# Performance work log

Hardware: AMD Instinct MI355X
Metric: run time of the kernel (lower is better)

Reference implementation:

```python
import jax, jax.numpy as jnp
import numpy as np

N, E, DIN, DH, DOUT, G, H = 40000, 400000, 256, 128, 128, 256, 4
BN_EPS = 1e-5      # nn.BatchNorm1d default
SM_EPS = 1e-16     # PyG softmax eps
NEG_SLOPE = 0.2    # GATConv default negative_slope


def _gat(x, src, dst, W, a_src, a_dst, b, heads, out_ch):
    # x:[N,Fin] W:[Fin,heads*out_ch] a_*:[heads,out_ch] b:[out_ch]
    n = x.shape[0]
    h = (x @ W).reshape(n, heads, out_ch)                     # [N,H,C]
    e = (h * a_src).sum(-1)[src] + (h * a_dst).sum(-1)[dst]   # [E,H] attention logits
    e = jnp.where(e > 0, e, NEG_SLOPE * e)                    # leaky_relu
    m = jax.ops.segment_max(e, dst, num_segments=n)           # segment softmax over incoming edges
    p = jnp.exp(e - m[dst])
    z = jax.ops.segment_sum(p, dst, num_segments=n)
    alpha = p / (z[dst] + SM_EPS)                             # [E,H]
    out = jax.ops.segment_sum(h[src] * alpha[:, :, None], dst, num_segments=n)  # [N,H,C]
    return out.mean(axis=1) + b                               # concat=False -> mean over heads, then bias


def _bn(x, g, b, m, v):
    # eval-mode BatchNorm1d with running stats
    return (x - m) * jax.lax.rsqrt(v + BN_EPS) * g + b


def setup_inputs():
    key = jax.random.key(0)
    ks = jax.random.split(key, 16)
    def rn(k, shape, fan):
        return jax.random.normal(k, shape, jnp.float32) / np.sqrt(fan).astype(np.float32)
    return {
        "x": jax.random.normal(ks[0], (N, DIN), jnp.float32),
        "src": jax.random.randint(ks[1], (E,), 0, N),
        "dst": jax.random.randint(ks[2], (E,), 0, N),
        "batch": jnp.sort(jax.random.randint(ks[3], (N,), 0, G)),
        "W1": rn(ks[4], (DIN, H * DH), DIN), "as1": rn(ks[5], (H, DH), DH), "ad1": rn(ks[6], (H, DH), DH), "b1": jnp.zeros((DH,), jnp.float32),
        "g1": jnp.ones((DH,), jnp.float32), "be1": jnp.zeros((DH,), jnp.float32), "m1": jnp.zeros((DH,), jnp.float32), "v1": jnp.ones((DH,), jnp.float32),
        "W2": rn(ks[7], (DH, H * DH), DH), "as2": rn(ks[8], (H, DH), DH), "ad2": rn(ks[9], (H, DH), DH), "b2": jnp.zeros((DH,), jnp.float32),
        "g2": jnp.ones((DH,), jnp.float32), "be2": jnp.zeros((DH,), jnp.float32), "m2": jnp.zeros((DH,), jnp.float32), "v2": jnp.ones((DH,), jnp.float32),
        "W3": rn(ks[10], (DH, DOUT), DH), "as3": rn(ks[11], (1, DOUT), DOUT), "ad3": rn(ks[12], (1, DOUT), DOUT), "b3": jnp.zeros((DOUT,), jnp.float32),
    }


def reference(x, src, dst, batch, W1, as1, ad1, b1, g1, be1, m1, v1,
              W2, as2, ad2, b2, g2, be2, m2, v2, W3, as3, ad3, b3):
    n = x.shape[0]
    loop = jnp.arange(n)
    s = jnp.concatenate([src, loop])  # PyG GATConv add_self_loops=True
    d = jnp.concatenate([dst, loop])
    h = jax.nn.elu(_gat(x, s, d, W1, as1, ad1, b1, H, DH))
    h = _bn(h, g1, be1, m1, v1)
    h = jax.nn.elu(_gat(h, s, d, W2, as2, ad2, b2, H, DH))
    h = _bn(h, g2, be2, m2, v2)
    h = _gat(h, s, d, W3, as3, ad3, b3, 1, DOUT)
    tot = jax.ops.segment_sum(h, batch, num_segments=G)      # global_mean_pool
    cnt = jax.ops.segment_sum(jnp.ones((n,), h.dtype), batch, num_segments=G)
    return tot / jnp.maximum(cnt, 1.0)[:, None]
```

## Files before the change

kernel.cpp:

```cpp
#include <hip/hip_runtime.h>
#include <cstdint>

#define N_NODES 40000
#define N_EDGES 400000
#define DIN 256
#define DHID 128
#define NG 256
#define NHEAD 4
#define ETOT (N_EDGES + N_NODES)

typedef __attribute__((ext_vector_type(8))) short short8;
typedef __attribute__((ext_vector_type(8))) unsigned short bfx8;
typedef __attribute__((ext_vector_type(4))) unsigned short bfx4;
typedef __attribute__((ext_vector_type(4))) float floatx4;

static __device__ __forceinline__ unsigned short f2bf(float f) {
    unsigned u = __float_as_uint(f);
    unsigned r = (u + 0x7FFFu + ((u >> 16) & 1u)) >> 16;
    return (unsigned short)r;
}
static __device__ __forceinline__ float bf2f(unsigned short s) {
    return __uint_as_float((unsigned)s << 16);
}


__global__ void count_kernel(const int* __restrict__ dst, int* __restrict__ deg) {
    int i = blockIdx.x * 256 + threadIdx.x;
    if (i >= ETOT) return;
    int d = (i < N_EDGES) ? dst[i] : (i - N_EDGES);
    atomicAdd(&deg[d], 1);
}

__global__ __launch_bounds__(1024) void scan_kernel(const int* __restrict__ deg,
                                                    int* __restrict__ offs,
                                                    int* __restrict__ cursor) {
    const int VPT = 40;
    __shared__ int wsum[16];
    int t = threadIdx.x;
    int lane = t & 63, wv = t >> 6;
    int base = t * VPT;
    int vals[VPT];
    int run = 0;
#pragma unroll
    for (int i = 0; i < VPT; i++) {
        int idx = base + i;
        int v = (idx < N_NODES) ? deg[idx] : 0;
        vals[i] = run;
        run += v;
    }
    int inc = run;
#pragma unroll
    for (int off = 1; off < 64; off <<= 1) {
        int n = __shfl_up(inc, off, 64);
        if (lane >= off) inc += n;
    }
    if (lane == 63) wsum[wv] = inc;
    __syncthreads();
    if (t == 0) {
        int c = 0;
#pragma unroll
        for (int i = 0; i < 16; i++) { int v = wsum[i]; wsum[i] = c; c += v; }
    }
    __syncthreads();
    int excl = wsum[wv] + inc - run;
#pragma unroll
    for (int i = 0; i < VPT; i++) {
        int idx = base + i;
        if (idx < N_NODES) { int o = excl + vals[i]; offs[idx] = o; cursor[idx] = o; }
    }
    if (t == 0) offs[N_NODES] = ETOT;
}

__global__ void fill_kernel(const int* __restrict__ src, const int* __restrict__ dst,
                            int* __restrict__ cursor, int* __restrict__ csr) {
    int i = blockIdx.x * 256 + threadIdx.x;
    if (i >= ETOT) return;
    int s, d;
    if (i < N_EDGES) { s = src[i]; d = dst[i]; } else { s = d = i - N_EDGES; }
    int pos = atomicAdd(&cursor[d], 1);
    csr[pos] = s;
}


__global__ void transpose_w_kernel(const float* __restrict__ W, unsigned short* __restrict__ Wt,
                                   int K, int Nn) {
    int i = blockIdx.x * 256 + threadIdx.x;
    if (i >= K * Nn) return;
    int k = i / Nn, n = i - k * Nn;
    Wt[(size_t)n * K + k] = f2bf(W[i]);
}


template <int K, int NCOL, bool AF32>
__global__ __launch_bounds__(256) void mfma_gemm_kernel(const void* __restrict__ Aptr,
                                                        const unsigned short* __restrict__ Bt,
                                                        unsigned short* __restrict__ C,
                                                        const float* __restrict__ asrc,
                                                        const float* __restrict__ adst,
                                                        float* __restrict__ ssrc,
                                                        float* __restrict__ sdst) {
    constexpr int KC = 128;
    constexpr int KP = KC + 8;
    constexpr int SH = NCOL / 128;
    __shared__ alignas(16) unsigned short A_lds[64][KP];
    __shared__ alignas(16) unsigned short B_lds[128][KP];

    const int tid = threadIdx.x;
    const int lane = tid & 63, wave = tid >> 6;
    const int row0 = blockIdx.x * 64;
    const int head = blockIdx.y;
    const int col0 = head * 128;
    const int cq = lane & 15, rq = lane >> 4;

    floatx4 acc[4][2] = {};

    for (int k0 = 0; k0 < K; k0 += KC) {
        if (k0) __syncthreads();
#pragma unroll
        for (int r = 0; r < 4; r++) {
            int i = r * 256 + tid;
            int row = i >> 4, slot = i & 15;
            if constexpr (AF32) {
                const float* ap = (const float*)Aptr + (size_t)(row0 + row) * K + k0 + slot * 8;
                float4 u0 = *(const float4*)ap;
                float4 u1 = *(const float4*)(ap + 4);
                short8 v;
                v[0] = (short)f2bf(u0.x); v[1] = (short)f2bf(u0.y);
                v[2] = (short)f2bf(u0.z); v[3] = (short)f2bf(u0.w);
                v[4] = (short)f2bf(u1.x); v[5] = (short)f2bf(u1.y);
                v[6] = (short)f2bf(u1.z); v[7] = (short)f2bf(u1.w);
                *(short8*)&A_lds[row][slot * 8] = v;
            } else {
                const unsigned short* ap = (const unsigned short*)Aptr + (size_t)(row0 + row) * K + k0 + slot * 8;
                *(short8*)&A_lds[row][slot * 8] = *(const short8*)ap;
            }
        }
#pragma unroll
        for (int r = 0; r < 8; r++) {
            int i = r * 256 + tid;
            int col = i >> 4, slot = i & 15;
            short8 v = *(const short8*)(Bt + (size_t)(col0 + col) * K + k0 + slot * 8);
            *(short8*)&B_lds[col][slot * 8] = v;
        }
        __syncthreads();

#pragma unroll
        for (int kk = 0; kk < KC; kk += 32) {
            short8 af[4], bfr[2];
#pragma unroll
            for (int i = 0; i < 4; i++)
                af[i] = *(const short8*)&A_lds[i * 16 + cq][kk + rq * 8];
#pragma unroll
            for (int j = 0; j < 2; j++)
                bfr[j] = *(const short8*)&B_lds[wave * 32 + j * 16 + cq][kk + rq * 8];
#pragma unroll
            for (int i = 0; i < 4; i++)
#pragma unroll
                for (int j = 0; j < 2; j++)
                    acc[i][j] = __builtin_amdgcn_mfma_f32_16x16x32_bf16(af[i], bfr[j], acc[i][j], 0, 0, 0);
        }
    }

#pragma unroll
    for (int i = 0; i < 4; i++)
#pragma unroll
        for (int j = 0; j < 2; j++) {
            unsigned short* cp = C + (size_t)(row0 + i * 16 + rq * 4) * NCOL + col0 + wave * 32 + j * 16 + cq;
#pragma unroll
            for (int r = 0; r < 4; r++)
                cp[(size_t)r * NCOL] = f2bf(acc[i][j][r]);
        }

    const float* ah = asrc + head * 128;
    const float* dh = adst + head * 128;
    float a0 = ah[wave * 32 + cq], a1 = ah[wave * 32 + 16 + cq];
    float d0 = dh[wave * 32 + cq], d1 = dh[wave * 32 + 16 + cq];

    __syncthreads();
    float* sred = (float*)&A_lds[0][0];
    float* dred = sred + 256;

#pragma unroll
    for (int i = 0; i < 4; i++)
#pragma unroll
        for (int r = 0; r < 4; r++) {
            float ss = acc[i][0][r] * a0 + acc[i][1][r] * a1;
            float sd = acc[i][0][r] * d0 + acc[i][1][r] * d1;
#pragma unroll
            for (int m = 1; m <= 8; m <<= 1) {
                ss += __shfl_xor(ss, m, 64);
                sd += __shfl_xor(sd, m, 64);
            }
            if (cq == 0) {
                int row = i * 16 + rq * 4 + r;
                sred[wave * 64 + row] = ss;
                dred[wave * 64 + row] = sd;
            }
        }
    __syncthreads();
    if (tid < 64) {
        float ss = sred[tid] + sred[64 + tid] + sred[128 + tid] + sred[192 + tid];
        float sd = dred[tid] + dred[64 + tid] + dred[128 + tid] + dred[192 + tid];
        ssrc[(size_t)(row0 + tid) * SH + head] = ss;
        sdst[(size_t)(row0 + tid) * SH + head] = sd;
    }
}


__global__ __launch_bounds__(256) void agg4_kernel(const int* __restrict__ offs,
                                                   const int* __restrict__ csr,
                                                   const unsigned short* __restrict__ hbuf,
                                                   const float4* __restrict__ ssrc4,
                                                   const float4* __restrict__ sdst4,
                                                   const float* __restrict__ bias,
                                                   const float* __restrict__ bng,
                                                   const float* __restrict__ bnb,
                                                   const float* __restrict__ bnm,
                                                   const float* __restrict__ bnv,
                                                   unsigned short* __restrict__ outb) {
    __shared__ alignas(16) float aload[4][64][4];
    __shared__ int sload[4][64];

    int wave = threadIdx.x >> 6, lane = threadIdx.x & 63;
    int d = blockIdx.x * 4 + wave;
    int off = offs[d];
    int deg = offs[d + 1] - off;
    int hh = lane >> 4;
    float4 sdv = sdst4[d];
    float acc[8] = {};

    if (deg <= 64) {
        int sreg = 0;
        float4 ev;
        if (lane < deg) {
            sreg = csr[off + lane];
            float4 es = ssrc4[sreg];
            ev.x = es.x + sdv.x; ev.x = ev.x > 0.f ? ev.x : 0.2f * ev.x;
            ev.y = es.y + sdv.y; ev.y = ev.y > 0.f ? ev.y : 0.2f * ev.y;
            ev.z = es.z + sdv.z; ev.z = ev.z > 0.f ? ev.z : 0.2f * ev.z;
            ev.w = es.w + sdv.w; ev.w = ev.w > 0.f ? ev.w : 0.2f * ev.w;
        } else { ev.x = ev.y = ev.z = ev.w = -1e30f; }
        float4 mx = ev;
#pragma unroll
        for (int m = 32; m >= 1; m >>= 1) {
            mx.x = fmaxf(mx.x, __shfl_xor(mx.x, m, 64));
            mx.y = fmaxf(mx.y, __shfl_xor(mx.y, m, 64));
            mx.z = fmaxf(mx.z, __shfl_xor(mx.z, m, 64));
            mx.w = fmaxf(mx.w, __shfl_xor(mx.w, m, 64));
        }
        float4 p;
        p.x = (lane < deg) ? __expf(ev.x - mx.x) : 0.f;
        p.y = (lane < deg) ? __expf(ev.y - mx.y) : 0.f;
        p.z = (lane < deg) ? __expf(ev.z - mx.z) : 0.f;
        p.w = (lane < deg) ? __expf(ev.w - mx.w) : 0.f;
        float4 z = p;
#pragma unroll
        for (int m = 32; m >= 1; m >>= 1) {
            z.x += __shfl_xor(z.x, m, 64);
            z.y += __shfl_xor(z.y, m, 64);
            z.z += __shfl_xor(z.z, m, 64);
            z.w += __shfl_xor(z.w, m, 64);
        }
        float4 alpha;
        alpha.x = p.x / (z.x + 1e-16f);
        alpha.y = p.y / (z.y + 1e-16f);
        alpha.z = p.z / (z.z + 1e-16f);
        alpha.w = p.w / (z.w + 1e-16f);

        *(float4*)&aload[wave][lane][0] = alpha;
        sload[wave][lane] = sreg;

        int j = 0;
        for (; j + 3 < deg; j += 4) {
            int s0 = sload[wave][j],     s1 = sload[wave][j + 1];
            int s2 = sload[wave][j + 2], s3 = sload[wave][j + 3];
            float a0 = aload[wave][j][hh],     a1 = aload[wave][j + 1][hh];
            float a2 = aload[wave][j + 2][hh], a3 = aload[wave][j + 3][hh];
            bfx8 v0 = *(const bfx8*)(hbuf + (size_t)s0 * 512 + lane * 8);
            bfx8 v1 = *(const bfx8*)(hbuf + (size_t)s1 * 512 + lane * 8);
            bfx8 v2 = *(const bfx8*)(hbuf + (size_t)s2 * 512 + lane * 8);
            bfx8 v3 = *(const bfx8*)(hbuf + (size_t)s3 * 512 + lane * 8);
#pragma unroll
            for (int i = 0; i < 8; i++)
                acc[i] += a0 * bf2f(v0[i]) + a1 * bf2f(v1[i]) +
                          a2 * bf2f(v2[i]) + a3 * bf2f(v3[i]);
        }
        for (; j < deg; j++) {
            int s = sload[wave][j];
            float a = aload[wave][j][hh];
            bfx8 hv = *(const bfx8*)(hbuf + (size_t)s * 512 + lane * 8);
#pragma unroll
            for (int i = 0; i < 8; i++) acc[i] += a * bf2f(hv[i]);
        }
    } else {
        float4 mx; mx.x = mx.y = mx.z = mx.w = -1e30f;
        for (int j = lane; j < deg; j += 64) {
            int s = csr[off + j];
            float4 es = ssrc4[s];
            float4 e;
            e.x = es.x + sdv.x; e.x = e.x > 0.f ? e.x : 0.2f * e.x;
            e.y = es.y + sdv.y; e.y = e.y > 0.f ? e.y : 0.2f * e.y;
            e.z = es.z + sdv.z; e.z = e.z > 0.f ? e.z : 0.2f * e.z;
            e.w = es.w + sdv.w; e.w = e.w > 0.f ? e.w : 0.2f * e.w;
            mx.x = fmaxf(mx.x, e.x); mx.y = fmaxf(mx.y, e.y);
            mx.z = fmaxf(mx.z, e.z); mx.w = fmaxf(mx.w, e.w);
        }
#pragma unroll
        for (int m = 32; m >= 1; m >>= 1) {
            mx.x = fmaxf(mx.x, __shfl_xor(mx.x, m, 64));
            mx.y = fmaxf(mx.y, __shfl_xor(mx.y, m, 64));
            mx.z = fmaxf(mx.z, __shfl_xor(mx.z, m, 64));
            mx.w = fmaxf(mx.w, __shfl_xor(mx.w, m, 64));
        }
        float4 z; z.x = z.y = z.z = z.w = 0.f;
        for (int j = lane; j < deg; j += 64) {
            int s = csr[off + j];
            float4 es = ssrc4[s];
            float4 e;
            e.x = es.x + sdv.x; e.x = e.x > 0.f ? e.x : 0.2f * e.x;
            e.y = es.y + sdv.y; e.y = e.y > 0.f ? e.y : 0.2f * e.y;
            e.z = es.z + sdv.z; e.z = e.z > 0.f ? e.z : 0.2f * e.z;
            e.w = es.w + sdv.w; e.w = e.w > 0.f ? e.w : 0.2f * e.w;
            z.x += __expf(e.x - mx.x); z.y += __expf(e.y - mx.y);
            z.z += __expf(e.z - mx.z); z.w += __expf(e.w - mx.w);
        }
#pragma unroll
        for (int m = 32; m >= 1; m >>= 1) {
            z.x += __shfl_xor(z.x, m, 64);
            z.y += __shfl_xor(z.y, m, 64);
            z.z += __shfl_xor(z.z, m, 64);
            z.w += __shfl_xor(z.w, m, 64);
        }
        float mc = hh == 0 ? mx.x : hh == 1 ? mx.y : hh == 2 ? mx.z : mx.w;
        float zc = hh == 0 ? z.x : hh == 1 ? z.y : hh == 2 ? z.z : z.w;
        float ic = 1.f / (zc + 1e-16f);
        float sdc = hh == 0 ? sdv.x : hh == 1 ? sdv.y : hh == 2 ? sdv.z : sdv.w;
        for (int j = 0; j < deg; j++) {
            int s = csr[off + j];
            float4 es = ssrc4[s];
            float ec = hh == 0 ? es.x : hh == 1 ? es.y : hh == 2 ? es.z : es.w;
            ec += sdc; ec = ec > 0.f ? ec : 0.2f * ec;
            float a = __expf(ec - mc) * ic;
            bfx8 hv = *(const bfx8*)(hbuf + (size_t)s * 512 + lane * 8);
#pragma unroll
            for (int i = 0; i < 8; i++) acc[i] += a * bf2f(hv[i]);
        }
    }

#pragma unroll
    for (int i = 0; i < 8; i++) {
        acc[i] += __shfl_xor(acc[i], 16, 64);
        acc[i] += __shfl_xor(acc[i], 32, 64);
    }
    if (lane < 16) {
        int c0 = lane * 8;
        bfx8 o;
#pragma unroll
        for (int i = 0; i < 8; i++) {
            int c = c0 + i;
            float v = acc[i] * 0.25f + bias[c];
            v = v > 0.f ? v : (__expf(v) - 1.0f);
            float sc = bng[c] * rsqrtf(bnv[c] + 1e-5f);
            v = (v - bnm[c]) * sc + bnb[c];
            o[i] = f2bf(v);
        }
        *(bfx8*)(outb + (size_t)d * 128 + c0) = o;
    }
}


__global__ __launch_bounds__(256) void agg1_kernel(const int* __restrict__ offs,
                                                   const int* __restrict__ csr,
                                                   const unsigned short* __restrict__ hbuf1,
                                                   const float* __restrict__ ssrc1,
                                                   const float* __restrict__ sdst1,
                                                   const float* __restrict__ bias,
                                                   float* __restrict__ h3out) {
    __shared__ float aload[4][64];
    __shared__ int sload[4][64];
    int wave = threadIdx.x >> 6, lane = threadIdx.x & 63;
    int d = blockIdx.x * 4 + wave;
    int off = offs[d];
    int deg = offs[d + 1] - off;
    int half = lane >> 5, li = lane & 31;
    float sdv = sdst1[d];
    float acc[4] = {};

    if (deg <= 64) {
        float ev = -1e30f; int sreg = 0;
        if (lane < deg) {
            sreg = csr[off + lane];
            ev = ssrc1[sreg] + sdv;
            ev = ev > 0.f ? ev : 0.2f * ev;
        }
        float mx = ev;
#pragma unroll
        for (int m = 32; m >= 1; m >>= 1) mx = fmaxf(mx, __shfl_xor(mx, m, 64));
        float p = (lane < deg) ? __expf(ev - mx) : 0.f;
        float z = p;
#pragma unroll
        for (int m = 32; m >= 1; m >>= 1) z += __shfl_xor(z, m, 64);
        aload[wave][lane] = p / (z + 1e-16f);
        sload[wave][lane] = sreg;

        int j = half;
        for (; j + 2 < deg; j += 4) {
            int s0 = sload[wave][j], s1 = sload[wave][j + 2];
            float a0 = aload[wave][j], a1 = aload[wave][j + 2];
            bfx4 v0 = *(const bfx4*)(hbuf1 + (size_t)s0 * 128 + li * 4);
            bfx4 v1 = *(const bfx4*)(hbuf1 + (size_t)s1 * 128 + li * 4);
#pragma unroll
            for (int i = 0; i < 4; i++)
                acc[i] += a0 * bf2f(v0[i]) + a1 * bf2f(v1[i]);
        }
        for (; j < deg; j += 2) {
            int s = sload[wave][j];
            float a = aload[wave][j];
            bfx4 hv = *(const bfx4*)(hbuf1 + (size_t)s * 128 + li * 4);
#pragma unroll
            for (int i = 0; i < 4; i++) acc[i] += a * bf2f(hv[i]);
        }
    } else {
        float mx = -1e30f;
        for (int j = lane; j < deg; j += 64) {
            float e = ssrc1[csr[off + j]] + sdv;
            e = e > 0.f ? e : 0.2f * e;
            mx = fmaxf(mx, e);
        }
#pragma unroll
        for (int m = 32; m >= 1; m >>= 1) mx = fmaxf(mx, __shfl_xor(mx, m, 64));
        float z = 0.f;
        for (int j = lane; j < deg; j += 64) {
            float e = ssrc1[csr[off + j]] + sdv;
            e = e > 0.f ? e : 0.2f * e;
            z += __expf(e - mx);
        }
#pragma unroll
        for (int m = 32; m >= 1; m >>= 1) z += __shfl_xor(z, m, 64);
        float inv = 1.f / (z + 1e-16f);
        for (int j = half; j < deg; j += 2) {
            int s = csr[off + j];
            float e = ssrc1[s] + sdv;
            e = e > 0.f ? e : 0.2f * e;
            float a = __expf(e - mx) * inv;
            bfx4 hv = *(const bfx4*)(hbuf1 + (size_t)s * 128 + li * 4);
#pragma unroll
            for (int i = 0; i < 4; i++) acc[i] += a * bf2f(hv[i]);
        }
    }

#pragma unroll
    for (int i = 0; i < 4; i++) acc[i] += __shfl_xor(acc[i], 32, 64);
    if (lane < 32) {
        float4 o;
        o.x = acc[0] + bias[li * 4];
        o.y = acc[1] + bias[li * 4 + 1];
        o.z = acc[2] + bias[li * 4 + 2];
        o.w = acc[3] + bias[li * 4 + 3];
        *(float4*)(h3out + (size_t)d * 128 + li * 4) = o;
    }
}


__global__ __launch_bounds__(256) void pool_kernel(const float* __restrict__ h3,
                                                   const int* __restrict__ batch,
                                                   float* __restrict__ out) {
    __shared__ float red[256];
    int g = blockIdx.x;
    int t = threadIdx.x;
    int lo = 0, n = N_NODES;
    while (n > 0) { int s = n >> 1; if (batch[lo + s] < g) { lo += s + 1; n -= s + 1; } else n = s; }
    int hi = lo; n = N_NODES - lo;
    while (n > 0) { int s = n >> 1; if (batch[hi + s] < g + 1) { hi += s + 1; n -= s + 1; } else n = s; }
    int c = t & 127;
    float acc = 0.f;
    for (int r = lo + (t >> 7); r < hi; r += 2)
        acc += h3[(size_t)r * 128 + c];
    red[t] = acc;
    __syncthreads();
    if (t < 128)
        out[(size_t)g * 128 + t] = (red[t] + red[t + 128]) / fmaxf((float)(hi - lo), 1.0f);
}


extern "C" void kernel_launch(void* const* d_in, const int* in_sizes, int n_in,
                              void* d_out, int out_size, void* d_ws, size_t ws_size,
                              hipStream_t stream) {
    const float* x    = (const float*)d_in[0];
    const int* src    = (const int*)d_in[1];
    const int* dst    = (const int*)d_in[2];
    const int* batch  = (const int*)d_in[3];
    const float* W1   = (const float*)d_in[4];
    const float* as1  = (const float*)d_in[5];
    const float* ad1  = (const float*)d_in[6];
    const float* b1   = (const float*)d_in[7];
    const float* g1   = (const float*)d_in[8];
    const float* be1  = (const float*)d_in[9];
    const float* m1   = (const float*)d_in[10];
    const float* v1   = (const float*)d_in[11];
    const float* W2   = (const float*)d_in[12];
    const float* as2  = (const float*)d_in[13];
    const float* ad2  = (const float*)d_in[14];
    const float* b2   = (const float*)d_in[15];
    const float* g2   = (const float*)d_in[16];
    const float* be2  = (const float*)d_in[17];
    const float* m2   = (const float*)d_in[18];
    const float* v2   = (const float*)d_in[19];
    const float* W3   = (const float*)d_in[20];
    const float* as3  = (const float*)d_in[21];
    const float* ad3  = (const float*)d_in[22];
    const float* b3   = (const float*)d_in[23];
    float* out = (float*)d_out;

    char* w = (char*)d_ws;
    size_t o = 0;
    auto alloc = [&](size_t bytes) -> void* {
        void* p = w + o;
        o += (bytes + 255) & ~(size_t)255;
        return p;
    };
    int* deg     = (int*)alloc((size_t)N_NODES * 4);
    int* offs    = (int*)alloc((size_t)(N_NODES + 1) * 4);
    int* cursor  = (int*)alloc((size_t)N_NODES * 4);
    int* csr     = (int*)alloc((size_t)ETOT * 4);
    float* ssrc  = (float*)alloc((size_t)N_NODES * NHEAD * 4);
    float* sdst  = (float*)alloc((size_t)N_NODES * NHEAD * 4);
    float* h3out = (float*)alloc((size_t)N_NODES * 128 * 4);
    unsigned short* hbuf = (unsigned short*)alloc((size_t)N_NODES * 512 * 2);
    unsigned short* xbuf = (unsigned short*)alloc((size_t)N_NODES * 128 * 2);
    unsigned short* W1t  = (unsigned short*)alloc((size_t)512 * 256 * 2);
    unsigned short* W2t  = (unsigned short*)alloc((size_t)512 * 128 * 2);
    unsigned short* W3t  = (unsigned short*)alloc((size_t)128 * 128 * 2);

    (void)hipMemsetAsync(deg, 0, (size_t)N_NODES * 4, stream);

    count_kernel<<<(ETOT + 255) / 256, 256, 0, stream>>>(dst, deg);
    scan_kernel<<<1, 1024, 0, stream>>>(deg, offs, cursor);
    fill_kernel<<<(ETOT + 255) / 256, 256, 0, stream>>>(src, dst, cursor, csr);

    transpose_w_kernel<<<(256 * 512 + 255) / 256, 256, 0, stream>>>(W1, W1t, 256, 512);
    transpose_w_kernel<<<(128 * 512 + 255) / 256, 256, 0, stream>>>(W2, W2t, 128, 512);
    transpose_w_kernel<<<(128 * 128 + 255) / 256, 256, 0, stream>>>(W3, W3t, 128, 128);

    mfma_gemm_kernel<256, 512, true><<<dim3(N_NODES / 64, 4), 256, 0, stream>>>(
        x, W1t, hbuf, as1, ad1, ssrc, sdst);
    agg4_kernel<<<N_NODES / 4, 256, 0, stream>>>(offs, csr, hbuf, (const float4*)ssrc,
                                                 (const float4*)sdst, b1, g1, be1, m1, v1, xbuf);

    mfma_gemm_kernel<128, 512, false><<<dim3(N_NODES / 64, 4), 256, 0, stream>>>(
        xbuf, W2t, hbuf, as2, ad2, ssrc, sdst);
    agg4_kernel<<<N_NODES / 4, 256, 0, stream>>>(offs, csr, hbuf, (const float4*)ssrc,
                                                 (const float4*)sdst, b2, g2, be2, m2, v2, xbuf);

    mfma_gemm_kernel<128, 128, false><<<dim3(N_NODES / 64, 1), 256, 0, stream>>>(
        xbuf, W3t, hbuf, as3, ad3, ssrc, sdst);
    agg1_kernel<<<N_NODES / 4, 256, 0, stream>>>(offs, csr, hbuf, ssrc, sdst, b3, h3out);

    pool_kernel<<<NG, 256, 0, stream>>>(h3out, batch, out);
}
```

Baseline: 486.1 us.

## Loop all heads inside GEMM block, fuse prep kernels, coalesce scan

The GEMM kernel now computes all heads in one block, looping over head column slabs, so the A tile (including the fp32→bf16 conversion for layer 1) is loaded once instead of once per head. The degree count and the three weight transposes are merged into a single prep kernel to cut launch count. The scan kernel is reorganised so each wave reads contiguous 64-element chunks in a coalesced way and does a per-chunk wave scan with a carry. In exchange, each GEMM block keeps four times as many accumulators and launches a quarter as many blocks, which may lower occupancy and parallelism.

```diff
diff --git a/kernel.cpp b/kernel.cpp
--- a/kernel.cpp
+++ b/kernel.cpp
@@ -24,37 +24,57 @@
 }
 
 
-__global__ void count_kernel(const int* __restrict__ dst, int* __restrict__ deg) {
-    int i = blockIdx.x * 256 + threadIdx.x;
-    if (i >= ETOT) return;
-    int d = (i < N_EDGES) ? dst[i] : (i - N_EDGES);
-    atomicAdd(&deg[d], 1);
-}
+#define NB_CNT 1719
+#define NB_W1  512
+#define NB_W2  256
+#define NB_W3  64
+
+__global__ void prep_kernel(const int* __restrict__ dst, int* __restrict__ deg,
+                            const float* __restrict__ W1, unsigned short* __restrict__ W1t,
+                            const float* __restrict__ W2, unsigned short* __restrict__ W2t,
+                            const float* __restrict__ W3, unsigned short* __restrict__ W3t) {
+    int b = blockIdx.x;
+    if (b < NB_CNT) {
+        int i = b * 256 + threadIdx.x;
+        if (i >= ETOT) return;
+        int d = (i < N_EDGES) ? dst[i] : (i - N_EDGES);
+        atomicAdd(&deg[d], 1);
+    } else if (b < NB_CNT + NB_W1) {
+        int i = (b - NB_CNT) * 256 + threadIdx.x;
+        int k = i >> 9, n = i & 511;
+        W1t[(size_t)n * 256 + k] = f2bf(W1[i]);
+    } else if (b < NB_CNT + NB_W1 + NB_W2) {
+        int i = (b - NB_CNT - NB_W1) * 256 + threadIdx.x;
+        int k = i >> 9, n = i & 511;
+        W2t[(size_t)n * 128 + k] = f2bf(W2[i]);
+    } else {
+        int i = (b - NB_CNT - NB_W1 - NB_W2) * 256 + threadIdx.x;
+        int k = i >> 7, n = i & 127;
+        W3t[(size_t)n * 128 + k] = f2bf(W3[i]);
+    }
+}
+
 
 __global__ __launch_bounds__(1024) void scan_kernel(const int* __restrict__ deg,
                                                     int* __restrict__ offs,
                                                     int* __restrict__ cursor) {
-    const int VPT = 40;
+    const int IT = 40;
     __shared__ int wsum[16];
     int t = threadIdx.x;
     int lane = t & 63, wv = t >> 6;
-    int base = t * VPT;
-    int vals[VPT];
-    int run = 0;
-#pragma unroll
-    for (int i = 0; i < VPT; i++) {
-        int idx = base + i;
+    int base = wv * 2560;
+    int vals[IT];
+    int lsum = 0;
+#pragma unroll
+    for (int i = 0; i < IT; i++) {
+        int idx = base + i * 64 + lane;
         int v = (idx < N_NODES) ? deg[idx] : 0;
-        vals[i] = run;
-        run += v;
-    }
-    int inc = run;
-#pragma unroll
-    for (int off = 1; off < 64; off <<= 1) {
-        int n = __shfl_up(inc, off, 64);
-        if (lane >= off) inc += n;
-    }
-    if (lane == 63) wsum[wv] = inc;
+        vals[i] = v;
+        lsum += v;
+    }
+#pragma unroll
+    for (int m = 32; m >= 1; m >>= 1) lsum += __shfl_xor(lsum, m, 64);
+    if (lane == 0) wsum[wv] = lsum;
     __syncthreads();
     if (t == 0) {
         int c = 0;
@@ -62,11 +82,20 @@
         for (int i = 0; i < 16; i++) { int v = wsum[i]; wsum[i] = c; c += v; }
     }
     __syncthreads();
-    int excl = wsum[wv] + inc - run;
-#pragma unroll
-    for (int i = 0; i < VPT; i++) {
-        int idx = base + i;
-        if (idx < N_NODES) { int o = excl + vals[i]; offs[idx] = o; cursor[idx] = o; }
+    int carry = wsum[wv];
+#pragma unroll
+    for (int i = 0; i < IT; i++) {
+        int v = vals[i];
+        int inc = v;
+#pragma unroll
+        for (int off = 1; off < 64; off <<= 1) {
+            int n = __shfl_up(inc, off, 64);
+            if (lane >= off) inc += n;
+        }
+        int tot = __shfl(inc, 63, 64);
+        int idx = base + i * 64 + lane;
+        if (idx < N_NODES) { int o = carry + inc - v; offs[idx] = o; cursor[idx] = o; }
+        carry += tot;
     }
     if (t == 0) offs[N_NODES] = ETOT;
 }
@@ -82,16 +111,7 @@
 }
 
 
-__global__ void transpose_w_kernel(const float* __restrict__ W, unsigned short* __restrict__ Wt,
-                                   int K, int Nn) {
-    int i = blockIdx.x * 256 + threadIdx.x;
-    if (i >= K * Nn) return;
-    int k = i / Nn, n = i - k * Nn;
-    Wt[(size_t)n * K + k] = f2bf(W[i]);
-}
-
-
-template <int K, int NCOL, bool AF32>
+template <int K, int SH, bool AF32>
 __global__ __launch_bounds__(256) void mfma_gemm_kernel(const void* __restrict__ Aptr,
                                                         const unsigned short* __restrict__ Bt,
                                                         unsigned short* __restrict__ C,
@@ -101,21 +121,19 @@
                                                         float* __restrict__ sdst) {
     constexpr int KC = 128;
     constexpr int KP = KC + 8;
-    constexpr int SH = NCOL / 128;
+    constexpr int NCOL = SH * 128;
     __shared__ alignas(16) unsigned short A_lds[64][KP];
     __shared__ alignas(16) unsigned short B_lds[128][KP];
 
     const int tid = threadIdx.x;
     const int lane = tid & 63, wave = tid >> 6;
     const int row0 = blockIdx.x * 64;
-    const int head = blockIdx.y;
-    const int col0 = head * 128;
     const int cq = lane & 15, rq = lane >> 4;
 
-    floatx4 acc[4][2] = {};
+    floatx4 acc[SH][4][2] = {};
 
     for (int k0 = 0; k0 < K; k0 += KC) {
-        if (k0) __syncthreads();
+        __syncthreads();
 #pragma unroll
         for (int r = 0; r < 4; r++) {
             int i = r * 256 + tid;
@@ -136,73 +154,79 @@
             }
         }
 #pragma unroll
-        for (int r = 0; r < 8; r++) {
-            int i = r * 256 + tid;
-            int col = i >> 4, slot = i & 15;
-            short8 v = *(const short8*)(Bt + (size_t)(col0 + col) * K + k0 + slot * 8);
-            *(short8*)&B_lds[col][slot * 8] = v;
-        }
-        __syncthreads();
-
-#pragma unroll
-        for (int kk = 0; kk < KC; kk += 32) {
-            short8 af[4], bfr[2];
-#pragma unroll
-            for (int i = 0; i < 4; i++)
-                af[i] = *(const short8*)&A_lds[i * 16 + cq][kk + rq * 8];
-#pragma unroll
-            for (int j = 0; j < 2; j++)
-                bfr[j] = *(const short8*)&B_lds[wave * 32 + j * 16 + cq][kk + rq * 8];
-#pragma unroll
-            for (int i = 0; i < 4; i++)
+        for (int h = 0; h < SH; h++) {
+            if (h) __syncthreads();
+#pragma unroll
+            for (int r = 0; r < 8; r++) {
+                int i = r * 256 + tid;
+                int col = i >> 4, slot = i & 15;
+                short8 v = *(const short8*)(Bt + (size_t)(h * 128 + col) * K + k0 + slot * 8);
+                *(short8*)&B_lds[col][slot * 8] = v;
+            }
+            __syncthreads();
+#pragma unroll
+            for (int kk = 0; kk < KC; kk += 32) {
+                short8 af[4], bfr[2];
+#pragma unroll
+                for (int i = 0; i < 4; i++)
+                    af[i] = *(const short8*)&A_lds[i * 16 + cq][kk + rq * 8];
 #pragma unroll
                 for (int j = 0; j < 2; j++)
-                    acc[i][j] = __builtin_amdgcn_mfma_f32_16x16x32_bf16(af[i], bfr[j], acc[i][j], 0, 0, 0);
-        }
-    }
-
-#pragma unroll
-    for (int i = 0; i < 4; i++)
-#pragma unroll
-        for (int j = 0; j < 2; j++) {
-            unsigned short* cp = C + (size_t)(row0 + i * 16 + rq * 4) * NCOL + col0 + wave * 32 + j * 16 + cq;
-#pragma unroll
-            for (int r = 0; r < 4; r++)
-                cp[(size_t)r * NCOL] = f2bf(acc[i][j][r]);
-        }
-
-    const float* ah = asrc + head * 128;
-    const float* dh = adst + head * 128;
-    float a0 = ah[wave * 32 + cq], a1 = ah[wave * 32 + 16 + cq];
-    float d0 = dh[wave * 32 + cq], d1 = dh[wave * 32 + 16 + cq];
-
-    __syncthreads();
+                    bfr[j] = *(const short8*)&B_lds[wave * 32 + j * 16 + cq][kk + rq * 8];
+#pragma unroll
+                for (int i = 0; i < 4; i++)
+#pragma unroll
+                    for (int j = 0; j < 2; j++)
+                        acc[h][i][j] = __builtin_amdgcn_mfma_f32_16x16x32_bf16(af[i], bfr[j], acc[h][i][j], 0, 0, 0);
+            }
+        }
+    }
+
+#pragma unroll
+    for (int h = 0; h < SH; h++)
+#pragma unroll
+        for (int i = 0; i < 4; i++)
+#pragma unroll
+            for (int j = 0; j < 2; j++) {
+                unsigned short* cp = C + (size_t)(row0 + i * 16 + rq * 4) * NCOL + h * 128 + wave * 32 + j * 16 + cq;
+#pragma unroll
+                for (int r = 0; r < 4; r++)
+                    cp[(size_t)r * NCOL] = f2bf(acc[h][i][j][r]);
+            }
+
     float* sred = (float*)&A_lds[0][0];
     float* dred = sred + 256;
-
-#pragma unroll
-    for (int i = 0; i < 4; i++)
-#pragma unroll
-        for (int r = 0; r < 4; r++) {
-            float ss = acc[i][0][r] * a0 + acc[i][1][r] * a1;
-            float sd = acc[i][0][r] * d0 + acc[i][1][r] * d1;
-#pragma unroll
-            for (int m = 1; m <= 8; m <<= 1) {
-                ss += __shfl_xor(ss, m, 64);
-                sd += __shfl_xor(sd, m, 64);
+#pragma unroll
+    for (int h = 0; h < SH; h++) {
+        const float* ah = asrc + h * 128;
+        const float* dh = adst + h * 128;
+        float a0 = ah[wave * 32 + cq], a1 = ah[wave * 32 + 16 + cq];
+        float d0 = dh[wave * 32 + cq], d1 = dh[wave * 32 + 16 + cq];
+        __syncthreads();
+#pragma unroll
+        for (int i = 0; i < 4; i++)
+#pragma unroll
+            for (int r = 0; r < 4; r++) {
+                float ss = acc[h][i][0][r] * a0 + acc[h][i][1][r] * a1;
+                float sd = acc[h][i][0][r] * d0 + acc[h][i][1][r] * d1;
+#pragma unroll
+                for (int m = 1; m <= 8; m <<= 1) {
+                    ss += __shfl_xor(ss, m, 64);
+                    sd += __shfl_xor(sd, m, 64);
+                }
+                if (cq == 0) {
+                    int row = i * 16 + rq * 4 + r;
+                    sred[wave * 64 + row] = ss;
+                    dred[wave * 64 + row] = sd;
+                }
             }
-            if (cq == 0) {
-                int row = i * 16 + rq * 4 + r;
-                sred[wave * 64 + row] = ss;
-                dred[wave * 64 + row] = sd;
-            }
-        }
-    __syncthreads();
-    if (tid < 64) {
-        float ss = sred[tid] + sred[64 + tid] + sred[128 + tid] + sred[192 + tid];
-        float sd = dred[tid] + dred[64 + tid] + dred[128 + tid] + dred[192 + tid];
-        ssrc[(size_t)(row0 + tid) * SH + head] = ss;
-        sdst[(size_t)(row0 + tid) * SH + head] = sd;
+        __syncthreads();
+        if (tid < 64) {
+            float ss = sred[tid] + sred[64 + tid] + sred[128 + tid] + sred[192 + tid];
+            float sd = dred[tid] + dred[64 + tid] + dred[128 + tid] + dred[192 + tid];
+            ssrc[(size_t)(row0 + tid) * SH + h] = ss;
+            sdst[(size_t)(row0 + tid) * SH + h] = sd;
+        }
     }
 }
 
@@ -534,25 +558,22 @@
 
     (void)hipMemsetAsync(deg, 0, (size_t)N_NODES * 4, stream);
 
-    count_kernel<<<(ETOT + 255) / 256, 256, 0, stream>>>(dst, deg);
+    prep_kernel<<<NB_CNT + NB_W1 + NB_W2 + NB_W3, 256, 0, stream>>>(
+        dst, deg, W1, W1t, W2, W2t, W3, W3t);
     scan_kernel<<<1, 1024, 0, stream>>>(deg, offs, cursor);
     fill_kernel<<<(ETOT + 255) / 256, 256, 0, stream>>>(src, dst, cursor, csr);
 
-    transpose_w_kernel<<<(256 * 512 + 255) / 256, 256, 0, stream>>>(W1, W1t, 256, 512);
-    transpose_w_kernel<<<(128 * 512 + 255) / 256, 256, 0, stream>>>(W2, W2t, 128, 512);
-    transpose_w_kernel<<<(128 * 128 + 255) / 256, 256, 0, stream>>>(W3, W3t, 128, 128);
-
-    mfma_gemm_kernel<256, 512, true><<<dim3(N_NODES / 64, 4), 256, 0, stream>>>(
+    mfma_gemm_kernel<256, 4, true><<<N_NODES / 64, 256, 0, stream>>>(
         x, W1t, hbuf, as1, ad1, ssrc, sdst);
     agg4_kernel<<<N_NODES / 4, 256, 0, stream>>>(offs, csr, hbuf, (const float4*)ssrc,
                                                  (const float4*)sdst, b1, g1, be1, m1, v1, xbuf);
 
-    mfma_gemm_kernel<128, 512, false><<<dim3(N_NODES / 64, 4), 256, 0, stream>>>(
+    mfma_gemm_kernel<128, 4, false><<<N_NODES / 64, 256, 0, stream>>>(
         xbuf, W2t, hbuf, as2, ad2, ssrc, sdst);
     agg4_kernel<<<N_NODES / 4, 256, 0, stream>>>(offs, csr, hbuf, (const float4*)ssrc,
                                                  (const float4*)sdst, b2, g2, be2, m2, v2, xbuf);
 
-    mfma_gemm_kernel<128, 128, false><<<dim3(N_NODES / 64, 1), 256, 0, stream>>>(
+    mfma_gemm_kernel<128, 1, false><<<N_NODES / 64, 256, 0, stream>>>(
         xbuf, W3t, hbuf, as3, ad3, ssrc, sdst);
     agg1_kernel<<<N_NODES / 4, 256, 0, stream>>>(offs, csr, hbuf, ssrc, sdst, b3, h3out);
 
```

After: 500.8 us. 1.03x slower.
